# Kernel tuning notes

Measured on AMD Instinct MI355X. Metric: run time of the kernel, lower is better.

The kernel has to match this reference:

```python
import jax, jax.numpy as jnp
import numpy as np

DIM, NH, HD = 1536, 12, 128
H, W, NFPB = 22, 40, 3
S = H * W * NFPB            # 2640 query tokens
PAST = 12 * H * W           # 10560 cached kv tokens
MAXF = 150                  # rope cache frames
EPS = 1e-6


def rmsnorm(y, g):
    # torch nn.RMSNorm over last dim
    return y * jax.lax.rsqrt(jnp.mean(y * y, axis=-1, keepdims=True) + EPS) * g


def build_rope_cache(freqs):
    # freqs: [MAXF, HD//2] angles -> flat (t,h,w) grid cache [MAXF*H*W, HD]
    hd2 = HD // 2               # 64
    c_h = hd2 // 3              # 21
    c_w = hd2 // 3              # 21
    c_t = hd2 - c_h - c_w       # 22
    f_t = freqs[:MAXF, :c_t]                       # [150, 22]
    f_h = freqs[:H, c_t:c_t + c_h]                 # [22, 21]
    f_w = freqs[:W, c_t + c_h:]                    # [40, 21]
    t_grid = jnp.broadcast_to(f_t[:, None, None, :], (MAXF, H, W, c_t))
    h_grid = jnp.broadcast_to(f_h[None, :, None, :], (MAXF, H, W, c_h))
    w_grid = jnp.broadcast_to(f_w[None, None, :, :], (MAXF, H, W, c_w))
    flat = jnp.concatenate([t_grid, h_grid, w_grid], -1).reshape(-1, hd2)
    return jnp.cos(flat), jnp.sin(flat)            # each [MAXF*H*W, 64]


def apply_rope_interleaved(t, cos, sin):
    # t: [s, n, HD]; cos/sin: [s, HD//2]; is_neox=False -> interleaved pairs
    te = t[..., 0::2]
    to = t[..., 1::2]
    c = cos[:, None, :]
    s = sin[:, None, :]
    oe = te * c - to * s
    oo = to * c + te * s
    return jnp.stack([oe, oo], axis=-1).reshape(t.shape)


def setup_inputs() -> dict:
    key = jax.random.key(0)
    ks = jax.random.split(key, 14)
    sc = 1.0 / np.sqrt(DIM)
    return {
        "x": jax.random.normal(ks[0], (1, S, DIM), jnp.float32),
        "freqs": jax.random.uniform(ks[1], (MAXF, HD // 2), jnp.float32),
        "cached_k": jax.random.normal(ks[2], (PAST, NH, HD), jnp.float32),
        "cached_v": jax.random.normal(ks[3], (PAST, NH, HD), jnp.float32),
        "Wq": jax.random.normal(ks[4], (DIM, DIM), jnp.float32) * sc,
        "bq": jax.random.normal(ks[5], (DIM,), jnp.float32) * 0.01,
        "Wk": jax.random.normal(ks[6], (DIM, DIM), jnp.float32) * sc,
        "bk": jax.random.normal(ks[7], (DIM,), jnp.float32) * 0.01,
        "Wv": jax.random.normal(ks[8], (DIM, DIM), jnp.float32) * sc,
        "bv": jax.random.normal(ks[9], (DIM,), jnp.float32) * 0.01,
        "Wo": jax.random.normal(ks[10], (DIM, DIM), jnp.float32) * sc,
        "bo": jax.random.normal(ks[11], (DIM,), jnp.float32) * 0.01,
        "gq": jnp.ones((DIM,), jnp.float32),
        "gk": jnp.ones((DIM,), jnp.float32),
        "current_start": PAST,
    }


def reference(x, freqs, cached_k, cached_v, Wq, bq, Wk, bk, Wv, bv, Wo, bo, gq, gk, current_start):
    xs = x[0]                                       # [S, DIM], B == 1
    q = rmsnorm(xs @ Wq.T + bq, gq).reshape(S, NH, HD)
    k = rmsnorm(xs @ Wk.T + bk, gk).reshape(S, NH, HD)
    v = (xs @ Wv.T + bv).reshape(S, NH, HD)

    cos_all, sin_all = build_rope_cache(freqs)
    pos = jnp.arange(S, dtype=jnp.int32) + current_start
    cos, sin = cos_all[pos], sin_all[pos]           # [S, 64]
    q = apply_rope_interleaved(q, cos, sin)
    k = apply_rope_interleaved(k, cos, sin)

    k_lin = jnp.concatenate([cached_k, k], axis=0)  # [KV, NH, HD]
    v_lin = jnp.concatenate([cached_v, v], axis=0)

    scale = 1.0 / np.sqrt(HD)
    scores = jnp.einsum("snd,knd->nsk", q, k_lin) * scale   # [NH, S, KV]
    probs = jax.nn.softmax(scores, axis=-1)
    out = jnp.einsum("nsk,knd->snd", probs, v_lin).reshape(S, DIM)
    return (out @ Wo.T + bo)[None]                  # [1, S, DIM]
```

## Files before the change

### kernel.cpp

```cpp
#include <hip/hip_runtime.h>

typedef unsigned short u16;
typedef short short8 __attribute__((ext_vector_type(8)));
typedef short short4b __attribute__((ext_vector_type(4)));
typedef float f32x4 __attribute__((ext_vector_type(4)));
typedef u16 us4 __attribute__((ext_vector_type(4)));
typedef unsigned u32x2 __attribute__((ext_vector_type(2)));

#define DIM   1536
#define NH    12
#define HD    128
#define SQ_   2640
#define SPAD  2688
#define PAST_ 10560
#define LTOT  13200
#define LPAD  13248

__device__ __forceinline__ u16 f2bf(float f){
  unsigned u = __builtin_bit_cast(unsigned, f);
  u += 0x7fffu + ((u >> 16) & 1u);
  return (u16)(u >> 16);
}
__device__ __forceinline__ float bf2f(u16 h){
  unsigned u = ((unsigned)h) << 16;
  return __builtin_bit_cast(float, u);
}
__device__ __forceinline__ unsigned cvtpk_bf16(float lo, float hi){
  unsigned r;
  asm("v_cvt_pk_bf16_f32 %0, %1, %2" : "=v"(r) : "v"(lo), "v"(hi));
  return r;
}
__device__ __forceinline__ void gload_lds16(const void* g, void* l){
  __builtin_amdgcn_global_load_lds(
      (const __attribute__((address_space(1))) void*)g,
      (__attribute__((address_space(3))) void*)l, 16, 0, 0);
}
__device__ __forceinline__ f32x4 mfma16(short4b a, short4b b, f32x4 c){
#if __has_builtin(__builtin_amdgcn_mfma_f32_16x16x16bf16_1k)
  return __builtin_amdgcn_mfma_f32_16x16x16bf16_1k(a, b, c, 0, 0, 0);
#else
  asm("v_mfma_f32_16x16x16_bf16 %0, %1, %2, %0" : "+v"(c) : "v"(a), "v"(b));
  return c;
#endif
}

__global__ void k_cvt(const float* __restrict__ s, u16* __restrict__ d, int n4){
  int i = blockIdx.x * 256 + threadIdx.x;
  if (i < n4){
    float4 f = ((const float4*)s)[i];
    us4 u; u[0]=f2bf(f.x); u[1]=f2bf(f.y); u[2]=f2bf(f.z); u[3]=f2bf(f.w);
    ((us4*)d)[i] = u;
  }
}

__global__ void k_prep_x(const float* __restrict__ x, u16* __restrict__ AB){
  int i = blockIdx.x * 256 + threadIdx.x;
  int e = i * 4;
  us4 u; u[0]=0; u[1]=0; u[2]=0; u[3]=0;
  if (e < SQ_*DIM){
    float4 f = ((const float4*)x)[i];
    u[0]=f2bf(f.x); u[1]=f2bf(f.y); u[2]=f2bf(f.z); u[3]=f2bf(f.w);
  }
  ((us4*)AB)[i] = u;
}

__global__ void k_prep_cache(const float* __restrict__ src, u16* __restrict__ dst, int n4){
  int i = blockIdx.x * 256 + threadIdx.x;
  if (i >= n4) return;
  int e = i * 4;
  if (e < PAST_*DIM){
    float4 f = ((const float4*)src)[i];
    us4 u; u[0]=f2bf(f.x); u[1]=f2bf(f.y); u[2]=f2bf(f.z); u[3]=f2bf(f.w);
    ((us4*)dst)[i] = u;
  } else {
    us4 u; u[0]=0; u[1]=0; u[2]=0; u[3]=0;
    ((us4*)dst)[i - PAST_*DIM/4 + LTOT*DIM/4] = u;
  }
}

__global__ void k_zero(u16* __restrict__ d, int n4){
  int i = blockIdx.x * 256 + threadIdx.x;
  if (i < n4){ us4 u; u[0]=0; u[1]=0; u[2]=0; u[3]=0; ((us4*)d)[i] = u; }
}

__global__ __launch_bounds__(256) void gemm_qkv(
  const u16* __restrict__ A,
  const u16* __restrict__ W0, const u16* __restrict__ W1, const u16* __restrict__ W2,
  const float* __restrict__ b0, const float* __restrict__ b1, const float* __restrict__ b2,
  u16* __restrict__ QL, u16* __restrict__ KL, u16* __restrict__ VA)
{
  __shared__ __align__(16) u16 As[4096];
  __shared__ __align__(16) u16 Bs[4096];
  int mt = blockIdx.x, nt = blockIdx.y;
  int tid = threadIdx.x, lane = tid & 63, w = tid >> 6;
  int wr = w >> 1, wc = w & 1;
  int which = nt / 12;
  const u16*  Bp = which==0 ? W0 : (which==1 ? W1 : W2);
  const float* bp = which==0 ? b0 : (which==1 ? b1 : b2);
  int nloc = (nt % 12) * 128;
  f32x4 acc[4][4];
  #pragma unroll
  for (int i=0;i<4;i++)
    #pragma unroll
    for (int j=0;j<4;j++) acc[i][j] = (f32x4){0.f,0.f,0.f,0.f};

  for (int k0 = 0; k0 < DIM; k0 += 32){
    #pragma unroll
    for (int p=0;p<2;p++){
      int e = (p*256 + tid) * 8;
      int r = e >> 5, c = e & 31;
      gload_lds16(A  + (size_t)(mt*128 + r)*DIM + k0 + c, (char*)As + p*4096 + (w<<10));
      gload_lds16(Bp + (size_t)(nloc   + r)*DIM + k0 + c, (char*)Bs + p*4096 + (w<<10));
    }
    __syncthreads();
    short8 af[4], bfr[4];
    #pragma unroll
    for (int i=0;i<4;i++){
      af[i]  = *(const short8*)&As[(wr*64 + i*16 + (lane&15))*32 + (lane>>4)*8];
      bfr[i] = *(const short8*)&Bs[(wc*64 + i*16 + (lane&15))*32 + (lane>>4)*8];
    }
    #pragma unroll
    for (int i=0;i<4;i++)
      #pragma unroll
      for (int j=0;j<4;j++)
        acc[i][j] = __builtin_amdgcn_mfma_f32_16x16x32_bf16(af[i], bfr[j], acc[i][j], 0,0,0);
    __syncthreads();
  }
  int rbase = mt*128 + wr*64;
  int cbase = nloc + wc*64;
  #pragma unroll
  for (int j=0;j<4;j++){
    int col = cbase + j*16 + (lane&15);
    float bb = bp[col];
    #pragma unroll
    for (int i=0;i<4;i++){
      #pragma unroll
      for (int q=0;q<4;q++){
        int row = rbase + i*16 + (lane>>4)*4 + q;
        if (row < SQ_){
          u16 uv = f2bf(acc[i][j][q] + bb);
          if (which==0)      QL[(size_t)row*DIM + col] = uv;
          else if (which==1) KL[(size_t)row*DIM + col] = uv;
          else               VA[(size_t)(PAST_ + row)*DIM + col] = uv;
        }
      }
    }
  }
}

__global__ __launch_bounds__(256) void gemm_out(
  const u16* __restrict__ A, const u16* __restrict__ W,
  const float* __restrict__ bias, float* __restrict__ out)
{
  __shared__ __align__(16) u16 As[4096];
  __shared__ __align__(16) u16 Bs[4096];
  int mt = blockIdx.x, nt = blockIdx.y;
  int tid = threadIdx.x, lane = tid & 63, w = tid >> 6;
  int wr = w >> 1, wc = w & 1;
  int nloc = nt * 128;
  f32x4 acc[4][4];
  #pragma unroll
  for (int i=0;i<4;i++)
    #pragma unroll
    for (int j=0;j<4;j++) acc[i][j] = (f32x4){0.f,0.f,0.f,0.f};

  for (int k0 = 0; k0 < DIM; k0 += 32){
    #pragma unroll
    for (int p=0;p<2;p++){
      int e = (p*256 + tid) * 8;
      int r = e >> 5, c = e & 31;
      gload_lds16(A + (size_t)(mt*128 + r)*DIM + k0 + c, (char*)As + p*4096 + (w<<10));
      gload_lds16(W + (size_t)(nloc   + r)*DIM + k0 + c, (char*)Bs + p*4096 + (w<<10));
    }
    __syncthreads();
    short8 af[4], bfr[4];
    #pragma unroll
    for (int i=0;i<4;i++){
      af[i]  = *(const short8*)&As[(wr*64 + i*16 + (lane&15))*32 + (lane>>4)*8];
      bfr[i] = *(const short8*)&Bs[(wc*64 + i*16 + (lane&15))*32 + (lane>>4)*8];
    }
    #pragma unroll
    for (int i=0;i<4;i++)
      #pragma unroll
      for (int j=0;j<4;j++)
        acc[i][j] = __builtin_amdgcn_mfma_f32_16x16x32_bf16(af[i], bfr[j], acc[i][j], 0,0,0);
    __syncthreads();
  }
  int rbase = mt*128 + wr*64;
  int cbase = nloc + wc*64;
  #pragma unroll
  for (int j=0;j<4;j++){
    int col = cbase + j*16 + (lane&15);
    float bb = bias[col];
    #pragma unroll
    for (int i=0;i<4;i++){
      #pragma unroll
      for (int q=0;q<4;q++){
        int row = rbase + i*16 + (lane>>4)*4 + q;
        if (row < SQ_) out[(size_t)row*DIM + col] = acc[i][j][q] + bb;
      }
    }
  }
}

__global__ __launch_bounds__(256) void norm_rope(
  const u16* __restrict__ QL, const u16* __restrict__ KL,
  const float* __restrict__ freqs, const float* __restrict__ gq, const float* __restrict__ gk,
  const int* __restrict__ cs,
  u16* __restrict__ Qout, u16* __restrict__ KAout)
{
  int s = blockIdx.x;
  int isk = blockIdx.y;
  int tid = threadIdx.x;
  const u16* src = (isk ? KL : QL) + (size_t)s*DIM + tid*6;
  float y[6];
  #pragma unroll
  for (int t=0;t<6;t++) y[t] = bf2f(src[t]);
  float ss = 0.f;
  #pragma unroll
  for (int t=0;t<6;t++) ss += y[t]*y[t];
  for (int mk=1; mk<64; mk<<=1) ss += __shfl_xor(ss, mk);
  __shared__ float red[4];
  if ((tid & 63) == 0) red[tid>>6] = ss;
  __syncthreads();
  float rn = rsqrtf((red[0]+red[1]+red[2]+red[3]) * (1.0f/1536.0f) + 1e-6f);
  rn *= isk ? 1.0f : 0.12752961954336302f;
  const float* g = (isk ? gk : gq) + tid*6;
  int pos = cs[0] + s;
  int tpos = pos / 880, rem = pos % 880;
  int hh = rem / 40, wp = rem % 40;
  u16 ov[6];
  #pragma unroll
  for (int pi=0; pi<3; pi++){
    int p = tid*3 + pi;
    int i = p & 63;
    int fr = (i < 22) ? tpos : ((i < 43) ? hh : wp);
    float ang = freqs[fr*64 + i];
    float sn, c;
    sincosf(ang, &sn, &c);
    float e  = y[pi*2]   * rn * g[pi*2];
    float od = y[pi*2+1] * rn * g[pi*2+1];
    ov[pi*2]   = f2bf(e*c - od*sn);
    ov[pi*2+1] = f2bf(od*c + e*sn);
  }
  u16* dst = isk ? (KAout + (size_t)(PAST_ + s)*DIM + tid*6)
                 : (Qout  + (size_t)s*DIM + tid*6);
  #pragma unroll
  for (int t=0;t<6;t++) dst[t] = ov[t];
}

__global__ __launch_bounds__(256, 2) void attn(
  const u16* __restrict__ Qf, const u16* __restrict__ KA,
  const u16* __restrict__ VA, u16* __restrict__ OP, float* __restrict__ ML)
{
  __shared__ __align__(16) u16 Ks[2][64*128];
  __shared__ __align__(16) u16 Vt[2][128*64];
  int h = blockIdx.y, qt = blockIdx.x, z = blockIdx.z;
  int tid = threadIdx.x, lane = tid & 63, w = tid >> 6;
  int g = lane >> 4, q = lane & 15;
  int qrow0 = qt*128 + w*32;
  int kvbeg = z ? 6656 : 0;
  int kvend = z ? LPAD : 6656;
  int c0 = (tid >> 4) << 3;
  int r0 = (tid & 15) << 2;

  short8 qa[2][4];
  #pragma unroll
  for (int cq=0;cq<2;cq++){
    const u16* qb = Qf + (size_t)(qrow0 + cq*16 + q)*DIM + h*HD + g*8;
    #pragma unroll
    for (int kt=0;kt<4;kt++) qa[cq][kt] = *(const short8*)(qb + kt*32);
  }
  f32x4 o[2][8];
  #pragma unroll
  for (int cq=0;cq<2;cq++)
    #pragma unroll
    for (int dt=0;dt<8;dt++) o[cq][dt] = (f32x4){0.f,0.f,0.f,0.f};
  float m[2] = {-1e30f,-1e30f};
  float l[2] = {0.f,0.f};

  auto stageK = [&](int kv0, u16* dK){
    #pragma unroll
    for (int p=0;p<4;p++){
      int e = w*2048 + p*512 + lane*8;
      int r = e >> 7;
      int bcol = (e & 127) << 1;
      int sb = bcol ^ ((r & 7) << 4);
      gload_lds16(KA + (size_t)(kv0 + r)*DIM + h*HD + (sb>>1),
                  (char*)dK + w*4096 + p*1024);
    }
  };
  auto loadV = [&](int kv0, short8* vr){
    const u16* vs = VA + (size_t)(kv0 + r0)*DIM + h*HD + c0;
    vr[0] = *(const short8*)(vs);
    vr[1] = *(const short8*)(vs + DIM);
    vr[2] = *(const short8*)(vs + 2*DIM);
    vr[3] = *(const short8*)(vs + 3*DIM);
  };
  auto writeVt = [&](u16* dV, short8* vr){
    #pragma unroll
    for (int j=0;j<8;j++){
      int d = c0 + j;
      int key = ((d & 7) << 4) | (((d >> 3) & 1) << 3);
      int off = d*128 + ((r0*2) ^ key);
      us4 pk; pk[0]=(u16)vr[0][j]; pk[1]=(u16)vr[1][j]; pk[2]=(u16)vr[2][j]; pk[3]=(u16)vr[3][j];
      *(us4*)((char*)dV + off) = pk;
    }
  };

  short8 vr[4];
  int cur = 0;
  stageK(kvbeg, &Ks[0][0]);
  loadV(kvbeg, vr);
  writeVt(&Vt[0][0], vr);
  __syncthreads();

  for (int kv0 = kvbeg; kv0 < kvend; kv0 += 64){
    int nxt = kv0 + 64;
    bool has_next = nxt < kvend;
    if (has_next){
      stageK(nxt, &Ks[cur^1][0]);
      loadV(nxt, vr);
    }
    f32x4 s4[2][4];
    #pragma unroll
    for (int cq=0;cq<2;cq++)
      #pragma unroll
      for (int ct=0;ct<4;ct++) s4[cq][ct] = (f32x4){0.f,0.f,0.f,0.f};
    const u16* ksb = &Ks[cur][0];
    #pragma unroll
    for (int ct=0;ct<4;ct++){
      int row = ct*16 + q;
      int rbyte = row*256, sw = (row & 7) << 4;
      #pragma unroll
      for (int kt=0;kt<4;kt++){
        int b = (kt*64 + (g<<4)) ^ sw;
        short8 kb = *(const short8*)((const char*)ksb + rbyte + b);
        s4[0][ct] = __builtin_amdgcn_mfma_f32_16x16x32_bf16(kb, qa[0][kt], s4[0][ct], 0,0,0);
        s4[1][ct] = __builtin_amdgcn_mfma_f32_16x16x32_bf16(kb, qa[1][kt], s4[1][ct], 0,0,0);
      }
    }
    if (kv0 + 64 > LTOT){
      #pragma unroll
      for (int ct=0;ct<4;ct++)
        #pragma unroll
        for (int j=0;j<4;j++)
          if (kv0 + ct*16 + g*4 + j >= LTOT){ s4[0][ct][j] = -1e30f; s4[1][ct][j] = -1e30f; }
    }
    float rm[2];
    #pragma unroll
    for (int cq=0;cq<2;cq++){
      float a0 = fmaxf(fmaxf(s4[cq][0][0], s4[cq][0][1]), s4[cq][0][2]);
      float a1 = fmaxf(fmaxf(s4[cq][0][3], s4[cq][1][0]), s4[cq][1][1]);
      float a2 = fmaxf(fmaxf(s4[cq][1][2], s4[cq][1][3]), s4[cq][2][0]);
      float a3 = fmaxf(fmaxf(s4[cq][2][1], s4[cq][2][2]), s4[cq][2][3]);
      float a4 = fmaxf(fmaxf(s4[cq][3][0], s4[cq][3][1]), s4[cq][3][2]);
      float r_ = fmaxf(fmaxf(a0, a1), fmaxf(fmaxf(a2, a3), fmaxf(a4, s4[cq][3][3])));
      r_ = fmaxf(r_, __shfl_xor(r_, 16));
      r_ = fmaxf(r_, __shfl_xor(r_, 32));
      rm[cq] = r_;
    }
    if (__any((rm[0] > m[0]+8.f) | (rm[1] > m[1]+8.f))){
      #pragma unroll
      for (int cq=0;cq<2;cq++){
        float mn = fmaxf(m[cq], rm[cq]);
        float al = exp2f(m[cq] - mn);
        m[cq] = mn;
        l[cq] *= al;
        #pragma unroll
        for (int dt=0;dt<8;dt++){
          f32x4 t = o[cq][dt];
          t[0]*=al; t[1]*=al; t[2]*=al; t[3]*=al;
          o[cq][dt] = t;
        }
      }
    }
    short4b pb[2][4];
    #pragma unroll
    for (int cq=0;cq<2;cq++){
      float rs = 0.f;
      #pragma unroll
      for (int ct=0;ct<4;ct++){
        float e0 = exp2f(s4[cq][ct][0] - m[cq]);
        float e1 = exp2f(s4[cq][ct][1] - m[cq]);
        float e2 = exp2f(s4[cq][ct][2] - m[cq]);
        float e3 = exp2f(s4[cq][ct][3] - m[cq]);
        rs += (e0 + e1) + (e2 + e3);
        u32x2 pw = { cvtpk_bf16(e0, e1), cvtpk_bf16(e2, e3) };
        pb[cq][ct] = __builtin_bit_cast(short4b, pw);
      }
      rs += __shfl_xor(rs, 16);
      rs += __shfl_xor(rs, 32);
      l[cq] += rs;
    }
    const u16* vtb = &Vt[cur][0];
    #pragma unroll
    for (int dt=0;dt<8;dt++){
      int d = dt*16 + q;
      int key = ((d & 7) << 4) | (((d >> 3) & 1) << 3);
      int rbyte = d*128;
      #pragma unroll
      for (int ct=0;ct<4;ct++){
        int b = (ct*32 + (g<<3)) ^ key;
        short4b va_ = *(const short4b*)((const char*)vtb + rbyte + b);
        o[0][dt] = mfma16(va_, pb[0][ct], o[0][dt]);
        o[1][dt] = mfma16(va_, pb[1][ct], o[1][dt]);
      }
    }
    if (has_next){
      writeVt(&Vt[cur^1][0], vr);
      __syncthreads();
      cur ^= 1;
    }
  }
  #pragma unroll
  for (int cq=0;cq<2;cq++){
    int row = qrow0 + cq*16 + q;
    size_t ob = ((size_t)(z*SPAD + row)*NH + h)*HD;
    #pragma unroll
    for (int dt=0;dt<8;dt++){
      u32x2 pw = { cvtpk_bf16(o[cq][dt][0], o[cq][dt][1]),
                   cvtpk_bf16(o[cq][dt][2], o[cq][dt][3]) };
      *(u32x2*)&OP[ob + dt*16 + g*4] = pw;
    }
    if (g == 0){
      size_t mb = ((size_t)(z*SPAD + row)*NH + h)*2;
      ML[mb] = m[cq]; ML[mb+1] = l[cq];
    }
  }
}

__global__ void merge_attn(const u16* __restrict__ OP, const float* __restrict__ ML,
                           u16* __restrict__ AB)
{
  int s = blockIdx.x, h = blockIdx.y, d = threadIdx.x;
  size_t i1 = ((size_t)s*NH + h)*2;
  size_t i2 = ((size_t)(SPAD + s)*NH + h)*2;
  float m1 = ML[i1], l1 = ML[i1+1];
  float m2 = ML[i2], l2 = ML[i2+1];
  float M = fmaxf(m1, m2);
  float e1 = exp2f(m1 - M), e2 = exp2f(m2 - M);
  float den = 1.0f / (l1*e1 + l2*e2);
  float o1 = bf2f(OP[((size_t)s*NH + h)*HD + d]);
  float o2 = bf2f(OP[((size_t)(SPAD + s)*NH + h)*HD + d]);
  AB[(size_t)s*DIM + h*HD + d] = f2bf((o1*e1 + o2*e2) * den);
}

extern "C" void kernel_launch(void* const* d_in, const int* in_sizes, int n_in,
                              void* d_out, int out_size, void* d_ws, size_t ws_size,
                              hipStream_t stream) {
  (void)in_sizes; (void)n_in; (void)out_size; (void)ws_size;
  const float* x    = (const float*)d_in[0];
  const float* freqs= (const float*)d_in[1];
  const float* ck   = (const float*)d_in[2];
  const float* cv   = (const float*)d_in[3];
  const float* Wq   = (const float*)d_in[4];
  const float* bq   = (const float*)d_in[5];
  const float* Wk   = (const float*)d_in[6];
  const float* bk   = (const float*)d_in[7];
  const float* Wv   = (const float*)d_in[8];
  const float* bv   = (const float*)d_in[9];
  const float* Wo   = (const float*)d_in[10];
  const float* bo   = (const float*)d_in[11];
  const float* gq   = (const float*)d_in[12];
  const float* gk   = (const float*)d_in[13];
  const int*   cs   = (const int*)d_in[14];
  float* out = (float*)d_out;
  char* ws = (char*)d_ws;

  u16* AB  = (u16*)(ws);
  u16* Wb3 = (u16*)(ws + 8257536);
  u16* QL  = (u16*)(ws + 12976128);
  u16* KA  = (u16*)(ws + 21233664);
  u16* VA  = (u16*)(ws + 61931520);
  u16* Wb0 = (u16*)(ws + 102629376);
  u16* Wb1 = (u16*)(ws + 107347968);
  u16* Wb2 = (u16*)(ws + 112066560);
  u16* KL  = (u16*)(ws + 116785152);
  u16*   OP = (u16*)(ws + 102629376);
  float* ML = (float*)(ws + 119144448);

  k_cvt<<<2304, 256, 0, stream>>>(Wq, Wb0, 589824);
  k_cvt<<<2304, 256, 0, stream>>>(Wk, Wb1, 589824);
  k_cvt<<<2304, 256, 0, stream>>>(Wv, Wb2, 589824);
  k_cvt<<<2304, 256, 0, stream>>>(Wo, Wb3, 589824);
  k_prep_x<<<4032, 256, 0, stream>>>(x, AB);
  k_prep_cache<<<15912, 256, 0, stream>>>(ck, KA, 4073472);
  k_prep_cache<<<15912, 256, 0, stream>>>(cv, VA, 4073472);
  k_zero<<<72, 256, 0, stream>>>(QL + (size_t)SQ_*DIM, 18432);

  gemm_qkv<<<dim3(21,36), 256, 0, stream>>>(AB, Wb0, Wb1, Wb2, bq, bk, bv, QL, KL, VA);
  norm_rope<<<dim3(2640,2), 256, 0, stream>>>(QL, KL, freqs, gq, gk, cs, QL, KA);
  attn<<<dim3(21,12,2), 256, 0, stream>>>(QL, KA, VA, OP, ML);
  merge_attn<<<dim3(2640,12), 128, 0, stream>>>(OP, ML, AB);
  gemm_out<<<dim3(21,12), 256, 0, stream>>>(AB, Wb3, bo, out);
}
```

Before: 533.4 us.

## Batch conversion launches, add MFMA priority hints, grid-stride merge kernel

The four weight-conversion launches become one 2D-grid kernel, and the K and V cache conversions become one launch, to cut launch overhead. The attention inner loops wrap their MFMA sections in s_setprio raises so matrix work on one wave gets issue priority over other waves' loads and softmax. The merge kernel changes from a 2640x12 grid of 128-thread blocks to a 2048-block grid-stride loop, which adds integer divides per element.

```diff
diff --git a/kernel.cpp b/kernel.cpp
--- a/kernel.cpp
+++ b/kernel.cpp
@@ -44,8 +44,14 @@
 #endif
 }
 
-__global__ void k_cvt(const float* __restrict__ s, u16* __restrict__ d, int n4){
+__global__ void k_cvt4(const float* __restrict__ s0, const float* __restrict__ s1,
+                       const float* __restrict__ s2, const float* __restrict__ s3,
+                       u16* __restrict__ d0, u16* __restrict__ d1,
+                       u16* __restrict__ d2, u16* __restrict__ d3, int n4){
   int i = blockIdx.x * 256 + threadIdx.x;
+  int y = blockIdx.y;
+  const float* s = (y==0)?s0:((y==1)?s1:((y==2)?s2:s3));
+  u16* d = (y==0)?d0:((y==1)?d1:((y==2)?d2:d3));
   if (i < n4){
     float4 f = ((const float4*)s)[i];
     us4 u; u[0]=f2bf(f.x); u[1]=f2bf(f.y); u[2]=f2bf(f.z); u[3]=f2bf(f.w);
@@ -64,9 +70,12 @@
   ((us4*)AB)[i] = u;
 }
 
-__global__ void k_prep_cache(const float* __restrict__ src, u16* __restrict__ dst, int n4){
+__global__ void k_prep_kv(const float* __restrict__ ck, const float* __restrict__ cv,
+                          u16* __restrict__ KA, u16* __restrict__ VA, int n4){
   int i = blockIdx.x * 256 + threadIdx.x;
   if (i >= n4) return;
+  const float* src = blockIdx.y ? cv : ck;
+  u16* dst = blockIdx.y ? VA : KA;
   int e = i * 4;
   if (e < PAST_*DIM){
     float4 f = ((const float4*)src)[i];
@@ -328,6 +337,7 @@
       #pragma unroll
       for (int ct=0;ct<4;ct++) s4[cq][ct] = (f32x4){0.f,0.f,0.f,0.f};
     const u16* ksb = &Ks[cur][0];
+    __builtin_amdgcn_s_setprio(1);
     #pragma unroll
     for (int ct=0;ct<4;ct++){
       int row = ct*16 + q;
@@ -340,6 +350,7 @@
         s4[1][ct] = __builtin_amdgcn_mfma_f32_16x16x32_bf16(kb, qa[1][kt], s4[1][ct], 0,0,0);
       }
     }
+    __builtin_amdgcn_s_setprio(0);
     if (kv0 + 64 > LTOT){
       #pragma unroll
       for (int ct=0;ct<4;ct++)
@@ -394,6 +405,7 @@
       l[cq] += rs;
     }
     const u16* vtb = &Vt[cur][0];
+    __builtin_amdgcn_s_setprio(1);
     #pragma unroll
     for (int dt=0;dt<8;dt++){
       int d = dt*16 + q;
@@ -407,6 +419,7 @@
         o[1][dt] = mfma16(va_, pb[1][ct], o[1][dt]);
       }
     }
+    __builtin_amdgcn_s_setprio(0);
     if (has_next){
       writeVt(&Vt[cur^1][0], vr);
       __syncthreads();
@@ -433,17 +446,23 @@
 __global__ void merge_attn(const u16* __restrict__ OP, const float* __restrict__ ML,
                            u16* __restrict__ AB)
 {
-  int s = blockIdx.x, h = blockIdx.y, d = threadIdx.x;
-  size_t i1 = ((size_t)s*NH + h)*2;
-  size_t i2 = ((size_t)(SPAD + s)*NH + h)*2;
-  float m1 = ML[i1], l1 = ML[i1+1];
-  float m2 = ML[i2], l2 = ML[i2+1];
-  float M = fmaxf(m1, m2);
-  float e1 = exp2f(m1 - M), e2 = exp2f(m2 - M);
-  float den = 1.0f / (l1*e1 + l2*e2);
-  float o1 = bf2f(OP[((size_t)s*NH + h)*HD + d]);
-  float o2 = bf2f(OP[((size_t)(SPAD + s)*NH + h)*HD + d]);
-  AB[(size_t)s*DIM + h*HD + d] = f2bf((o1*e1 + o2*e2) * den);
+  const int total = SQ_ * NH * HD;
+  for (int e = blockIdx.x * 256 + threadIdx.x; e < total; e += gridDim.x * 256){
+    int s = e / (NH*HD);
+    int r = e - s*(NH*HD);
+    int h = r >> 7;
+    int d = r & 127;
+    size_t i1 = ((size_t)s*NH + h)*2;
+    size_t i2 = ((size_t)(SPAD + s)*NH + h)*2;
+    float m1 = ML[i1], l1 = ML[i1+1];
+    float m2 = ML[i2], l2 = ML[i2+1];
+    float M = fmaxf(m1, m2);
+    float e1 = exp2f(m1 - M), e2 = exp2f(m2 - M);
+    float den = 1.0f / (l1*e1 + l2*e2);
+    float o1 = bf2f(OP[((size_t)s*NH + h)*HD + d]);
+    float o2 = bf2f(OP[((size_t)(SPAD + s)*NH + h)*HD + d]);
+    AB[(size_t)s*DIM + h*HD + d] = f2bf((o1*e1 + o2*e2) * den);
+  }
 }
 
 extern "C" void kernel_launch(void* const* d_in, const int* in_sizes, int n_in,
@@ -480,18 +499,14 @@
   u16*   OP = (u16*)(ws + 102629376);
   float* ML = (float*)(ws + 119144448);
 
-  k_cvt<<<2304, 256, 0, stream>>>(Wq, Wb0, 589824);
-  k_cvt<<<2304, 256, 0, stream>>>(Wk, Wb1, 589824);
-  k_cvt<<<2304, 256, 0, stream>>>(Wv, Wb2, 589824);
-  k_cvt<<<2304, 256, 0, stream>>>(Wo, Wb3, 589824);
+  k_cvt4<<<dim3(2304,4), 256, 0, stream>>>(Wq, Wk, Wv, Wo, Wb0, Wb1, Wb2, Wb3, 589824);
   k_prep_x<<<4032, 256, 0, stream>>>(x, AB);
-  k_prep_cache<<<15912, 256, 0, stream>>>(ck, KA, 4073472);
-  k_prep_cache<<<15912, 256, 0, stream>>>(cv, VA, 4073472);
+  k_prep_kv<<<dim3(15912,2), 256, 0, stream>>>(ck, cv, KA, VA, 4073472);
   k_zero<<<72, 256, 0, stream>>>(QL + (size_t)SQ_*DIM, 18432);
 
   gemm_qkv<<<dim3(21,36), 256, 0, stream>>>(AB, Wb0, Wb1, Wb2, bq, bk, bv, QL, KL, VA);
   norm_rope<<<dim3(2640,2), 256, 0, stream>>>(QL, KL, freqs, gq, gk, cs, QL, KA);
   attn<<<dim3(21,12,2), 256, 0, stream>>>(QL, KA, VA, OP, ML);
-  merge_attn<<<dim3(2640,12), 128, 0, stream>>>(OP, ML, AB);
+  merge_attn<<<2048, 256, 0, stream>>>(OP, ML, AB);
   gemm_out<<<dim3(21,12), 256, 0, stream>>>(AB, Wb3, bo, out);
 }
```

Measured after the change: 521.3 us. 1.02x faster.
